# Kernel tuning notes

Measured on AMD Instinct MI355X. Metric: run time of the kernel, lower is better.

The kernel has to match this reference:

```python
import jax, jax.numpy as jnp
import numpy as np

B, S, H = 32, 2048, 1024  # S == MAX_LENGTH
SIGMA = 1.0


def setup_inputs() -> dict:
    key = jax.random.key(0)
    k1, k2, k3, k4 = jax.random.split(key, 4)
    return {
        "encoder_outputs": jax.random.normal(k1, (B, S, H), dtype=jnp.float32),
        "decoder_hidden": jax.random.normal(k2, (B, H), dtype=jnp.float32),
        "timestep": jax.random.randint(k3, (B,), 0, S, dtype=jnp.int32),
        # 0.02 scale keeps align scores in a sane range so softmax is not saturated
        "Wa_w": jax.random.normal(k4, (H, H), dtype=jnp.float32) * 0.02,
        "Wa_b": jnp.zeros((H,), dtype=jnp.float32),
    }


def reference(encoder_outputs, decoder_hidden, timestep, Wa_w, Wa_b):
    # method='monotonic', align_method='general'
    b, s_len, h = encoder_outputs.shape

    # align 'general': scores[b,s] = dec[b] . (Wa @ enc[b,s])  (torch Linear: x @ W^T + b)
    keys = jnp.einsum('bsh,dh->bsd', encoder_outputs, Wa_w) + Wa_b  # [B,S,H]
    scores = jnp.einsum('bh,bsh->bs', decoder_hidden, keys)          # [B,S]

    # monotonic: p_t = timestep, gaussian window centered at p_t
    s = jnp.arange(s_len, dtype=jnp.float32)                          # [S]
    p_t = timestep.astype(jnp.float32)[:, None]                       # [B,1]
    gaussian = jnp.exp(-((s[None, :] - p_t) ** 2) / (2.0 * SIGMA ** 2))  # [B,S]

    attn = jax.nn.softmax(scores, axis=1) * gaussian                  # [B,S]
    context = jnp.einsum('bs,bsh->bh', attn, encoder_outputs)         # [B,H]
    return context, attn
```

## Files before the change

### kernel.cpp

```cpp
#include <hip/hip_runtime.h>

#define NB 32
#define NS 2048
#define NH 1024
#define WIN 15

__global__ __launch_bounds__(256) void k1_v(const float* __restrict__ dec,
                                            const float* __restrict__ Wa,
                                            float* __restrict__ v,
                                            double* __restrict__ denomD,
                                            float* __restrict__ ctx) {
    __shared__ float red[256];
    int blk = blockIdx.x;
    int b = blk & 31, ht = blk >> 5;
    int t = threadIdx.x;
    if (blk == 0 && t < NB) denomD[t] = 0.0;
    if (blk < 128) ctx[blk * 256 + t] = 0.f;

    int ds = t >> 6, hl = t & 63;
    int h = ht * 64 + hl;
    const float* decb = dec + b * NH + ds * 256;
    const float* wa   = Wa + (size_t)(ds * 256) * NH + h;
    float a0 = 0.f, a1 = 0.f, a2 = 0.f, a3 = 0.f;
#pragma unroll 2
    for (int d = 0; d < 256; d += 4) {
        a0 = fmaf(decb[d],     wa[(size_t)d * NH],       a0);
        a1 = fmaf(decb[d + 1], wa[(size_t)(d + 1) * NH], a1);
        a2 = fmaf(decb[d + 2], wa[(size_t)(d + 2) * NH], a2);
        a3 = fmaf(decb[d + 3], wa[(size_t)(d + 3) * NH], a3);
    }
    red[t] = (a0 + a1) + (a2 + a3);
    __syncthreads();
    if (t < 64)
        v[b * NH + ht * 64 + t] = red[t] + red[t + 64] + red[t + 128] + red[t + 192];
}

__global__ __launch_bounds__(256) void k2_scores(const float* __restrict__ enc,
                                                 const float* __restrict__ v,
                                                 float* __restrict__ scores,
                                                 double* __restrict__ denomD) {
    __shared__ float vs[NH];
    __shared__ float rowsc[16];
    int t = threadIdx.x, wid = t >> 6, lane = t & 63;
    int b = blockIdx.x >> 7;
    int row0 = blockIdx.x << 4;

    ((float4*)vs)[t] = ((const float4*)(v + b * NH))[t];
    __syncthreads();
    const float4* vv = (const float4*)vs;
    float4 vr0 = vv[lane], vr1 = vv[64 + lane], vr2 = vv[128 + lane], vr3 = vv[192 + lane];

    int r0 = row0 + wid * 4;
    const float4* eb = (const float4*)(enc + (size_t)r0 * NH);
    float acc[4];
#pragma unroll
    for (int r = 0; r < 4; ++r) {
        float4 x0 = eb[r * 256 + lane];
        float4 x1 = eb[r * 256 + 64 + lane];
        float4 x2 = eb[r * 256 + 128 + lane];
        float4 x3 = eb[r * 256 + 192 + lane];
        float s = 0.f;
        s = fmaf(x0.x, vr0.x, s); s = fmaf(x0.y, vr0.y, s);
        s = fmaf(x0.z, vr0.z, s); s = fmaf(x0.w, vr0.w, s);
        s = fmaf(x1.x, vr1.x, s); s = fmaf(x1.y, vr1.y, s);
        s = fmaf(x1.z, vr1.z, s); s = fmaf(x1.w, vr1.w, s);
        s = fmaf(x2.x, vr2.x, s); s = fmaf(x2.y, vr2.y, s);
        s = fmaf(x2.z, vr2.z, s); s = fmaf(x2.w, vr2.w, s);
        s = fmaf(x3.x, vr3.x, s); s = fmaf(x3.y, vr3.y, s);
        s = fmaf(x3.z, vr3.z, s); s = fmaf(x3.w, vr3.w, s);
        acc[r] = s;
    }
#pragma unroll
    for (int r = 0; r < 4; ++r) {
        float s = acc[r];
#pragma unroll
        for (int off = 32; off >= 1; off >>= 1) s += __shfl_xor(s, off, 64);
        if (lane == 0) { scores[r0 + r] = s; rowsc[wid * 4 + r] = s; }
    }
    __syncthreads();
    if (t < 16) {
        double e = exp((double)rowsc[t]);
#pragma unroll
        for (int off = 8; off >= 1; off >>= 1) e += __shfl_xor(e, off, 64);
        if (t == 0) atomicAdd(&denomD[b], e);
    }
}

__global__ __launch_bounds__(256) void k3_out(const float* __restrict__ enc,
                                              const float* __restrict__ scores,
                                              const int* __restrict__ ts,
                                              const double* __restrict__ denomD,
                                              float* __restrict__ ctx,
                                              float* __restrict__ attn) {
    int b = blockIdx.x >> 3;
    int c = blockIdx.x & 7;
    int t = threadIdx.x;

    float lse = (float)log(denomD[b]);
    int p = ts[b];
    float pf = (float)p;

    int s = c * 256 + t;
    float sc = scores[b * NS + s];
    float d = (float)s - pf;
    attn[(size_t)b * NS + s] = expf(sc - lse - 0.5f * d * d);

    int w0 = max(0, p - WIN), w1 = min(NS - 1, p + WIN);
    int r0 = max(w0, c * 256), r1 = min(w1, c * 256 + 255);
    if (r0 <= r1) {
        const float* sb = scores + (size_t)b * NS;
        float a0 = 0.f, a1 = 0.f, a2 = 0.f, a3 = 0.f;
        for (int r = r0; r <= r1; ++r) {
            float dr = (float)r - pf;
            float w = expf(sb[r] - lse - 0.5f * dr * dr);
            const float* er = enc + ((size_t)b * NS + r) * NH;
            a0 = fmaf(w, er[t],       a0);
            a1 = fmaf(w, er[t + 256], a1);
            a2 = fmaf(w, er[t + 512], a2);
            a3 = fmaf(w, er[t + 768], a3);
        }
        atomicAdd(&ctx[b * NH + t],       a0);
        atomicAdd(&ctx[b * NH + t + 256], a1);
        atomicAdd(&ctx[b * NH + t + 512], a2);
        atomicAdd(&ctx[b * NH + t + 768], a3);
    }
}

extern "C" void kernel_launch(void* const* d_in, const int* in_sizes, int n_in,
                              void* d_out, int out_size, void* d_ws, size_t ws_size,
                              hipStream_t stream) {
    const float* enc  = (const float*)d_in[0];
    const float* dec  = (const float*)d_in[1];
    const int*   ts   = (const int*)d_in[2];
    const float* Wa_w = (const float*)d_in[3];

    float* out  = (float*)d_out;
    float* ctx  = out;
    float* attn = out + NB * NH;

    float*  v      = (float*)d_ws;
    float*  scores = v + NB * NH;
    double* denomD = (double*)(scores + NB * NS);

    k1_v     <<<512,  256, 0, stream>>>(dec, Wa_w, v, denomD, ctx);
    k2_scores<<<4096, 256, 0, stream>>>(enc, v, scores, denomD);
    k3_out   <<<NB*8, 256, 0, stream>>>(enc, scores, ts, denomD, ctx, attn);
}
```

Measured before the change: 77.99 us.

## Fuse softmax/context epilogue into scores kernel via last-block completion counter

Merges the third kernel into the scores kernel. A per-batch atomic counter picks the last block to finish, and that block computes the full attn row and the windowed context directly. This removes one kernel launch, the ctx zeroing and the ctx atomics. In exchange, the epilogue for each batch is serialized onto a single block at the tail, and correctness now depends on threadfence ordering for the cross-block reads of scores and denom.

Measured after the change: 267.7 us. 243% more time.

```diff
diff --git a/kernel.cpp b/kernel.cpp
--- a/kernel.cpp
+++ b/kernel.cpp
@@ -9,13 +9,12 @@
                                             const float* __restrict__ Wa,
                                             float* __restrict__ v,
                                             double* __restrict__ denomD,
-                                            float* __restrict__ ctx) {
+                                            int* __restrict__ done) {
     __shared__ float red[256];
     int blk = blockIdx.x;
     int b = blk & 31, ht = blk >> 5;
     int t = threadIdx.x;
-    if (blk == 0 && t < NB) denomD[t] = 0.0;
-    if (blk < 128) ctx[blk * 256 + t] = 0.f;
+    if (blk == 0 && t < NB) { denomD[t] = 0.0; done[t] = 0; }
 
     int ds = t >> 6, hl = t & 63;
     int h = ht * 64 + hl;
@@ -35,12 +34,17 @@
         v[b * NH + ht * 64 + t] = red[t] + red[t + 64] + red[t + 128] + red[t + 192];
 }
 
-__global__ __launch_bounds__(256) void k2_scores(const float* __restrict__ enc,
-                                                 const float* __restrict__ v,
-                                                 float* __restrict__ scores,
-                                                 double* __restrict__ denomD) {
+__global__ __launch_bounds__(256) void k2_fused(const float* __restrict__ enc,
+                                                const float* __restrict__ v,
+                                                const int* __restrict__ ts,
+                                                float* __restrict__ scores,
+                                                double* __restrict__ denomD,
+                                                int* __restrict__ done,
+                                                float* __restrict__ ctx,
+                                                float* __restrict__ attn) {
     __shared__ float vs[NH];
     __shared__ float rowsc[16];
+    __shared__ int winner;
     int t = threadIdx.x, wid = t >> 6, lane = t & 63;
     int b = blockIdx.x >> 7;
     int row0 = blockIdx.x << 4;
@@ -78,51 +82,47 @@
         if (lane == 0) { scores[r0 + r] = s; rowsc[wid * 4 + r] = s; }
     }
     __syncthreads();
+
     if (t < 16) {
         double e = exp((double)rowsc[t]);
 #pragma unroll
         for (int off = 8; off >= 1; off >>= 1) e += __shfl_xor(e, off, 64);
-        if (t == 0) atomicAdd(&denomD[b], e);
+        if (t == 0) {
+            atomicAdd(&denomD[b], e);
+            __threadfence();
+            int old = atomicAdd(&done[b], 1);
+            winner = (old == 127) ? 1 : 0;
+        }
     }
-}
+    __syncthreads();
 
-__global__ __launch_bounds__(256) void k3_out(const float* __restrict__ enc,
-                                              const float* __restrict__ scores,
-                                              const int* __restrict__ ts,
-                                              const double* __restrict__ denomD,
-                                              float* __restrict__ ctx,
-                                              float* __restrict__ attn) {
-    int b = blockIdx.x >> 3;
-    int c = blockIdx.x & 7;
-    int t = threadIdx.x;
-
-    float lse = (float)log(denomD[b]);
-    int p = ts[b];
-    float pf = (float)p;
-
-    int s = c * 256 + t;
-    float sc = scores[b * NS + s];
-    float d = (float)s - pf;
-    attn[(size_t)b * NS + s] = expf(sc - lse - 0.5f * d * d);
-
-    int w0 = max(0, p - WIN), w1 = min(NS - 1, p + WIN);
-    int r0 = max(w0, c * 256), r1 = min(w1, c * 256 + 255);
-    if (r0 <= r1) {
+    if (winner) {
+        __threadfence();
+        float lse = (float)log(denomD[b]);
+        int p = ts[b];
+        float pf = (float)p;
         const float* sb = scores + (size_t)b * NS;
-        float a0 = 0.f, a1 = 0.f, a2 = 0.f, a3 = 0.f;
-        for (int r = r0; r <= r1; ++r) {
+#pragma unroll
+        for (int k = 0; k < 8; ++k) {
+            int s = t + 256 * k;
+            float d = (float)s - pf;
+            attn[(size_t)b * NS + s] = expf(sb[s] - lse - 0.5f * d * d);
+        }
+        int w0 = max(0, p - WIN), w1 = min(NS - 1, p + WIN);
+        float c0 = 0.f, c1 = 0.f, c2 = 0.f, c3 = 0.f;
+        for (int r = w0; r <= w1; ++r) {
             float dr = (float)r - pf;
             float w = expf(sb[r] - lse - 0.5f * dr * dr);
             const float* er = enc + ((size_t)b * NS + r) * NH;
-            a0 = fmaf(w, er[t],       a0);
-            a1 = fmaf(w, er[t + 256], a1);
-            a2 = fmaf(w, er[t + 512], a2);
-            a3 = fmaf(w, er[t + 768], a3);
+            c0 = fmaf(w, er[t],       c0);
+            c1 = fmaf(w, er[t + 256], c1);
+            c2 = fmaf(w, er[t + 512], c2);
+            c3 = fmaf(w, er[t + 768], c3);
         }
-        atomicAdd(&ctx[b * NH + t],       a0);
-        atomicAdd(&ctx[b * NH + t + 256], a1);
-        atomicAdd(&ctx[b * NH + t + 512], a2);
-        atomicAdd(&ctx[b * NH + t + 768], a3);
+        ctx[b * NH + t]       = c0;
+        ctx[b * NH + t + 256] = c1;
+        ctx[b * NH + t + 512] = c2;
+        ctx[b * NH + t + 768] = c3;
     }
 }
 
@@ -141,8 +141,8 @@
     float*  v      = (float*)d_ws;
     float*  scores = v + NB * NH;
     double* denomD = (double*)(scores + NB * NS);
+    int*    done   = (int*)(denomD + NB);
 
-    k1_v     <<<512,  256, 0, stream>>>(dec, Wa_w, v, denomD, ctx);
-    k2_scores<<<4096, 256, 0, stream>>>(enc, v, scores, denomD);
-    k3_out   <<<NB*8, 256, 0, stream>>>(enc, scores, ts, denomD, ctx, attn);
+    k1_v    <<<512,  256, 0, stream>>>(dec, Wa_w, v, denomD, done);
+    k2_fused<<<4096, 256, 0, stream>>>(enc, v, ts, scores, denomD, done, ctx, attn);
 }
```
